# Performance work log

Measured on AMD Instinct MI355X. Metric: run time of the kernel, lower is better.

The kernel has to match this reference:

```python
import jax, jax.numpy as jnp
import numpy as np

N, D, M, E, K = 16384, 512, 1024, 8, 2
LOSS_COEF = 0.01
EPS = 1e-10


def setup_inputs() -> dict:
    key = jax.random.key(0)
    ks = jax.random.split(key, 6)
    x = jax.random.normal(ks[0], (N, D), dtype=jnp.float32)
    # gate weight (torch init is zeros; use small random so routing is non-degenerate)
    w_gate = 0.02 * jax.random.normal(ks[1], (D, E), dtype=jnp.float32)
    # stacked expert FFN params: Linear(D->M), GELU, Linear(M->D)
    W1 = jax.random.normal(ks[2], (E, D, M), dtype=jnp.float32) / np.sqrt(D)
    b1 = jnp.zeros((E, M), dtype=jnp.float32)
    W2 = jax.random.normal(ks[3], (E, M, D), dtype=jnp.float32) / np.sqrt(M)
    b2 = jnp.zeros((E, D), dtype=jnp.float32)
    return {"x": x, "w_gate": w_gate, "W1": W1, "b1": b1, "W2": W2, "b2": b2}


def _cv_squared(v):
    # torch .var() is unbiased (ddof=1)
    v = v.astype(jnp.float32)
    return jnp.var(v, ddof=1) / (jnp.mean(v) ** 2 + EPS)


def reference(x, w_gate, W1, b1, W2, b2):
    n = x.shape[0]
    # --- noisy_top_k_gating (eval path: no noise) ---
    logits = x @ w_gate                                  # [N, E]
    top_logits, top_idx = jax.lax.top_k(logits, min(K + 1, E))
    topk_logits = top_logits[:, :K]                      # [N, K]
    topk_idx = top_idx[:, :K]                            # [N, K]
    topk_gates = jax.nn.softmax(topk_logits, axis=-1)    # [N, K]
    gates = jnp.zeros_like(logits).at[jnp.arange(n)[:, None], topk_idx].set(topk_gates)
    importance = gates.sum(axis=0)                       # [E]
    load = (gates > 0).sum(axis=0).astype(jnp.float32)   # [E]
    loss = LOSS_COEF * (_cv_squared(importance) + _cv_squared(load))
    # --- experts (dense equivalent of sparse dispatch/combine: gate==0 rows contribute 0) ---
    h = jnp.einsum('nd,edm->enm', x, W1) + b1[:, None, :]     # [E, N, M]
    h = jax.nn.gelu(h, approximate=False)
    out = jnp.einsum('enm,emd->end', h, W2) + b2[:, None, :]  # [E, N, D]
    y = jnp.einsum('ne,end->nd', gates, out)                  # [N, D]
    return (y, loss)
```

## Files before the change

kernel.cpp:

```cpp
#include <hip/hip_runtime.h>
#include <math.h>

#define NTOK 16384
#define DDIM 512
#define MDIM 1024
#define NEXP 8
#define LDSW 32
#define TMAX 264

typedef __attribute__((ext_vector_type(8))) short short8;
typedef __attribute__((ext_vector_type(4))) float floatx4;

__device__ inline unsigned short f2bf(float f){
  union { float f; unsigned int u; } v; v.f = f;
  unsigned int u = v.u;
  u += ((u >> 16) & 1u) + 0x7fffu;
  return (unsigned short)(u >> 16);
}

__device__ inline float bf2f(unsigned short s){
  union { unsigned int u; float f; } v;
  v.u = ((unsigned int)s) << 16;
  return v.f;
}

__device__ inline float gelu_fast(float x){
  float u = x * 0.70710678118654752f;
  float a = fabsf(u);
  float t = __builtin_amdgcn_rcpf(fmaf(0.3275911f, a, 1.0f));
  float p = fmaf(1.061405429f, t, -1.453152027f);
  p = fmaf(p, t, 1.421413741f);
  p = fmaf(p, t, -0.284496736f);
  p = fmaf(p, t, 0.254829592f);
  p = p * t;
  float e = __expf(-u * u);
  float erfa = fmaf(-p, e, 1.0f);
  float erfu = copysignf(erfa, u);
  return 0.5f * x * (1.0f + erfu);
}

__device__ __forceinline__ void gload16(const unsigned short* g, unsigned short* l){
  __builtin_amdgcn_global_load_lds(
      (const __attribute__((address_space(1))) void*)g,
      (__attribute__((address_space(3))) void*)l,
      16, 0, 0);
}


__global__ void init_small_kernel(int* counts, float* imp){
  int t = threadIdx.x;
  if (t < NEXP){ counts[t] = 0; imp[t] = 0.0f; }
}

__global__ void transpose_conv_kernel(const float* __restrict__ in,
                                      unsigned short* __restrict__ out,
                                      int R, int C){
  __shared__ float tile[32][33];
  int e  = blockIdx.z;
  int c0 = blockIdx.x << 5;
  int r0 = blockIdx.y << 5;
  const float* src = in + (size_t)e * R * C;
  unsigned short* dst = out + (size_t)e * R * C;
  int tc = threadIdx.x;
  int tr = threadIdx.y;
  #pragma unroll
  for (int i = 0; i < 32; i += 8)
    tile[tr + i][tc] = src[(size_t)(r0 + tr + i) * C + c0 + tc];
  __syncthreads();
  #pragma unroll
  for (int i = 0; i < 32; i += 8)
    dst[(size_t)(c0 + tr + i) * R + r0 + tc] = f2bf(tile[tc][tr + i]);
}


__global__ __launch_bounds__(256)
void gating_kernel(const float* __restrict__ x,
                   const float* __restrict__ wg,
                   unsigned short* __restrict__ xb,
                   int* __restrict__ tok_e, float* __restrict__ tok_g,
                   int* __restrict__ counts, float* __restrict__ imp){
  __shared__ int   lcnt[NEXP];
  __shared__ float limp[NEXP];
  int t = threadIdx.x;
  if (t < NEXP){ lcnt[t] = 0; limp[t] = 0.0f; }
  __syncthreads();

  int wave = t >> 6;
  int lane = t & 63;

  for (int it = 0; it < 16; it++){
    int n = blockIdx.x * 64 + it * 4 + wave;

    const float4* xp = (const float4*)(x + (size_t)n * DDIM + lane * 8);
    float4 a = xp[0], b = xp[1];
    float xv[8] = {a.x, a.y, a.z, a.w, b.x, b.y, b.z, b.w};

    short8 xo;
    #pragma unroll
    for (int j = 0; j < 8; j++) xo[j] = (short)f2bf(xv[j]);
    *(short8*)(xb + (size_t)n * DDIM + lane * 8) = xo;

    double acc[NEXP];
    #pragma unroll
    for (int e = 0; e < NEXP; e++) acc[e] = 0.0;
    #pragma unroll
    for (int j = 0; j < 8; j++){
      const float* wr = wg + (size_t)(lane * 8 + j) * NEXP;
      #pragma unroll
      for (int e = 0; e < NEXP; e++) acc[e] += (double)xv[j] * (double)wr[e];
    }
    #pragma unroll
    for (int off = 32; off >= 1; off >>= 1){
      #pragma unroll
      for (int e = 0; e < NEXP; e++) acc[e] += __shfl_xor(acc[e], off);
    }
    if (lane == 0){
      int i0 = -1, i1 = -1;
      double l0 = -1e300, l1 = -1e300;
      #pragma unroll
      for (int e = 0; e < NEXP; e++){
        double v = acc[e];
        if (v > l0){ l1 = l0; i1 = i0; l0 = v; i0 = e; }
        else if (v > l1){ l1 = v; i1 = e; }
      }
      float ex = expf((float)(l1 - l0));
      float g0 = 1.0f / (1.0f + ex);
      float g1 = ex / (1.0f + ex);
      tok_e[n * 2]     = i0; tok_e[n * 2 + 1] = i1;
      tok_g[n * 2]     = g0; tok_g[n * 2 + 1] = g1;
      atomicAdd(&lcnt[i0], 1); atomicAdd(&lcnt[i1], 1);
      atomicAdd(&limp[i0], g0); atomicAdd(&limp[i1], g1);
    }
  }
  __syncthreads();
  if (t < NEXP){
    atomicAdd(&counts[t], lcnt[t]);
    atomicAdd(&imp[t], limp[t]);
  }
}

__global__ void loss_scan_kernel(const int* __restrict__ counts,
                                 const float* __restrict__ imp,
                                 int* __restrict__ offsets, int* __restrict__ cursor,
                                 int* __restrict__ tile_pre,
                                 float* __restrict__ out_loss){
  int off = 0, tp = 0;
  double si = 0, si2 = 0, sl = 0, sl2 = 0;
  for (int e = 0; e < NEXP; e++){
    offsets[e] = off; cursor[e] = off;
    tile_pre[e] = tp;
    tp += (counts[e] + 127) >> 7;
    off += counts[e];
    double im = (double)imp[e];
    double ld = (double)counts[e];
    si += im; si2 += im * im;
    sl += ld; sl2 += ld * ld;
  }
  offsets[NEXP] = off;
  tile_pre[NEXP] = tp;
  double mi = si / 8.0, ml = sl / 8.0;
  double vi = (si2 - 8.0 * mi * mi) / 7.0;
  double vl = (sl2 - 8.0 * ml * ml) / 7.0;
  double loss = 0.01 * (vi / (mi * mi + 1e-10) + vl / (ml * ml + 1e-10));
  *out_loss = (float)loss;
}

__global__ __launch_bounds__(256)
void scatter_kernel(const int* __restrict__ tok_e,
                    int* __restrict__ cursor,
                    int* __restrict__ btok, int* __restrict__ slot_of){
  __shared__ int lcnt[NEXP];
  __shared__ int lbase[NEXP];
  int t = threadIdx.x;
  if (t < NEXP) lcnt[t] = 0;
  __syncthreads();

  int n = blockIdx.x * 256 + t;
  int e0 = tok_e[n * 2], e1 = tok_e[n * 2 + 1];
  int r0 = atomicAdd(&lcnt[e0], 1);
  int r1 = atomicAdd(&lcnt[e1], 1);
  __syncthreads();
  if (t < NEXP) lbase[t] = atomicAdd(&cursor[t], lcnt[t]);
  __syncthreads();
  int s0 = lbase[e0] + r0;
  int s1 = lbase[e1] + r1;
  btok[s0] = n;
  btok[s1] = n;
  slot_of[n * 2]     = s0;
  slot_of[n * 2 + 1] = s1;
}


__global__ __launch_bounds__(256)
void gemm1_kernel(const unsigned short* __restrict__ xb,
                  const unsigned short* __restrict__ w1t,
                  const float* __restrict__ b1,
                  const int* __restrict__ offsets,
                  const int* __restrict__ tile_pre,
                  const int* __restrict__ btok,
                  unsigned short* __restrict__ H){
  int ct = blockIdx.x / TMAX;
  int tt = blockIdx.x % TMAX;
  if (tt >= tile_pre[NEXP]) return;
  int e = 0;
  while (tt >= tile_pre[e + 1]) e++;
  int rt = tt - tile_pre[e];
  int off = offsets[e];
  int cnt = offsets[e + 1] - off;
  int r0 = rt << 7;

  __shared__ unsigned short As[128 * LDSW];
  __shared__ unsigned short Bs[128 * LDSW];

  int t = threadIdx.x;
  int srow = t >> 2;
  int scol = (t & 3) << 3;
  int w = t >> 6;

  int ra0 = r0 + srow;        if (ra0 >= cnt) ra0 = cnt - 1;
  int ra1 = r0 + 64 + srow;   if (ra1 >= cnt) ra1 = cnt - 1;
  const unsigned short* aptr0 = xb + (size_t)btok[off + ra0] * DDIM + scol;
  const unsigned short* aptr1 = xb + (size_t)btok[off + ra1] * DDIM + scol;
  const unsigned short* bptr0 = w1t + ((size_t)e * MDIM + (ct << 7) + srow) * DDIM + scol;
  const unsigned short* bptr1 = bptr0 + (size_t)64 * DDIM;

  unsigned short* As0 = As + w * 512;
  unsigned short* As1 = As + 2048 + w * 512;
  unsigned short* Bs0 = Bs + w * 512;
  unsigned short* Bs1 = Bs + 2048 + w * 512;

  int lane = t & 63;
  int wr = (w >> 1) << 6;
  int wc = (w & 1) << 6;
  int lm = lane & 15;
  int lq = lane >> 4;

  const unsigned short* Ar[4];
  const unsigned short* Br[4];
  #pragma unroll
  for (int i = 0; i < 4; i++){
    Ar[i] = &As[(wr + i * 16 + lm) * LDSW + lq * 8];
    Br[i] = &Bs[(wc + i * 16 + lm) * LDSW + lq * 8];
  }

  floatx4 acc[4][4] = {};
  for (int k0 = 0; k0 < DDIM; k0 += 32){
    gload16(aptr0 + k0, As0);
    gload16(aptr1 + k0, As1);
    gload16(bptr0 + k0, Bs0);
    gload16(bptr1 + k0, Bs1);
    __syncthreads();
    short8 af[4], bf[4];
    #pragma unroll
    for (int i = 0; i < 4; i++) af[i] = *(const short8*)Ar[i];
    #pragma unroll
    for (int j = 0; j < 4; j++) bf[j] = *(const short8*)Br[j];
    #pragma unroll
    for (int i = 0; i < 4; i++)
      #pragma unroll
      for (int j = 0; j < 4; j++)
        acc[i][j] = __builtin_amdgcn_mfma_f32_16x16x32_bf16(af[i], bf[j], acc[i][j], 0, 0, 0);
    __syncthreads();
  }

  const float* bias = b1 + e * MDIM + (ct << 7);
  #pragma unroll
  for (int i = 0; i < 4; i++){
    int rbase = wr + i * 16 + lq * 4;
    #pragma unroll
    for (int j = 0; j < 4; j++){
      int cc = wc + j * 16 + lm;
      float bv = bias[cc];
      #pragma unroll
      for (int r = 0; r < 4; r++){
        int row = r0 + rbase + r;
        if (row < cnt){
          float v = acc[i][j][r] + bv;
          H[(size_t)(off + row) * MDIM + (ct << 7) + cc] = f2bf(gelu_fast(v));
        }
      }
    }
  }
}

__global__ __launch_bounds__(256)
void gemm2_kernel(const unsigned short* __restrict__ H,
                  const unsigned short* __restrict__ w2t,
                  const float* __restrict__ b2,
                  const int* __restrict__ offsets,
                  const int* __restrict__ tile_pre,
                  unsigned short* __restrict__ O){
  int ct = blockIdx.x / TMAX;
  int tt = blockIdx.x % TMAX;
  if (tt >= tile_pre[NEXP]) return;
  int e = 0;
  while (tt >= tile_pre[e + 1]) e++;
  int rt = tt - tile_pre[e];
  int off = offsets[e];
  int cnt = offsets[e + 1] - off;
  int r0 = rt << 7;

  __shared__ unsigned short As[128 * LDSW];
  __shared__ unsigned short Bs[128 * LDSW];

  int t = threadIdx.x;
  int srow = t >> 2;
  int scol = (t & 3) << 3;
  int w = t >> 6;

  int ra0 = r0 + srow;        if (ra0 >= cnt) ra0 = cnt - 1;
  int ra1 = r0 + 64 + srow;   if (ra1 >= cnt) ra1 = cnt - 1;
  const unsigned short* aptr0 = H + (size_t)(off + ra0) * MDIM + scol;
  const unsigned short* aptr1 = H + (size_t)(off + ra1) * MDIM + scol;
  const unsigned short* bptr0 = w2t + ((size_t)e * DDIM + (ct << 7) + srow) * MDIM + scol;
  const unsigned short* bptr1 = bptr0 + (size_t)64 * MDIM;

  unsigned short* As0 = As + w * 512;
  unsigned short* As1 = As + 2048 + w * 512;
  unsigned short* Bs0 = Bs + w * 512;
  unsigned short* Bs1 = Bs + 2048 + w * 512;

  int lane = t & 63;
  int wr = (w >> 1) << 6;
  int wc = (w & 1) << 6;
  int lm = lane & 15;
  int lq = lane >> 4;

  const unsigned short* Ar[4];
  const unsigned short* Br[4];
  #pragma unroll
  for (int i = 0; i < 4; i++){
    Ar[i] = &As[(wr + i * 16 + lm) * LDSW + lq * 8];
    Br[i] = &Bs[(wc + i * 16 + lm) * LDSW + lq * 8];
  }

  floatx4 acc[4][4] = {};
  for (int k0 = 0; k0 < MDIM; k0 += 32){
    gload16(aptr0 + k0, As0);
    gload16(aptr1 + k0, As1);
    gload16(bptr0 + k0, Bs0);
    gload16(bptr1 + k0, Bs1);
    __syncthreads();
    short8 af[4], bf[4];
    #pragma unroll
    for (int i = 0; i < 4; i++) af[i] = *(const short8*)Ar[i];
    #pragma unroll
    for (int j = 0; j < 4; j++) bf[j] = *(const short8*)Br[j];
    #pragma unroll
    for (int i = 0; i < 4; i++)
      #pragma unroll
      for (int j = 0; j < 4; j++)
        acc[i][j] = __builtin_amdgcn_mfma_f32_16x16x32_bf16(af[i], bf[j], acc[i][j], 0, 0, 0);
    __syncthreads();
  }

  const float* bias = b2 + e * DDIM + (ct << 7);
  #pragma unroll
  for (int i = 0; i < 4; i++){
    int rbase = wr + i * 16 + lq * 4;
    #pragma unroll
    for (int j = 0; j < 4; j++){
      int cc = wc + j * 16 + lm;
      float bv = bias[cc];
      #pragma unroll
      for (int r = 0; r < 4; r++){
        int row = r0 + rbase + r;
        if (row < cnt)
          O[(size_t)(off + row) * DDIM + (ct << 7) + cc] = f2bf(acc[i][j][r] + bv);
      }
    }
  }
}


__global__ __launch_bounds__(256)
void combine_kernel(const unsigned short* __restrict__ O,
                    const float* __restrict__ tok_g,
                    const int* __restrict__ slot_of,
                    float* __restrict__ y){
  int wave = threadIdx.x >> 6;
  int lane = threadIdx.x & 63;
  int n = blockIdx.x * 4 + wave;
  int s0 = slot_of[n * 2], s1 = slot_of[n * 2 + 1];
  float g0 = tok_g[n * 2], g1 = tok_g[n * 2 + 1];
  short8 a = *(const short8*)(O + (size_t)s0 * DDIM + lane * 8);
  short8 b = *(const short8*)(O + (size_t)s1 * DDIM + lane * 8);
  float4 o0, o1;
  float* po0 = (float*)&o0;
  float* po1 = (float*)&o1;
  #pragma unroll
  for (int j = 0; j < 4; j++){
    po0[j] = g0 * bf2f((unsigned short)a[j]) + g1 * bf2f((unsigned short)b[j]);
    po1[j] = g0 * bf2f((unsigned short)a[j + 4]) + g1 * bf2f((unsigned short)b[j + 4]);
  }
  float4* yp = (float4*)(y + (size_t)n * DDIM + lane * 8);
  yp[0] = o0;
  yp[1] = o1;
}


extern "C" void kernel_launch(void* const* d_in, const int* in_sizes, int n_in,
                              void* d_out, int out_size, void* d_ws, size_t ws_size,
                              hipStream_t stream){
  const float* x  = (const float*)d_in[0];
  const float* wg = (const float*)d_in[1];
  const float* W1 = (const float*)d_in[2];
  const float* b1 = (const float*)d_in[3];
  const float* W2 = (const float*)d_in[4];
  const float* b2 = (const float*)d_in[5];
  float* y = (float*)d_out;

  char* ws = (char*)d_ws;
  size_t o = 0;
  auto alloc = [&](size_t bytes)->char*{
    char* p = ws + o;
    o += (bytes + 255) & ~(size_t)255;
    return p;
  };
  unsigned short* xb   = (unsigned short*)alloc((size_t)NTOK * DDIM * 2);
  unsigned short* w1t  = (unsigned short*)alloc((size_t)NEXP * MDIM * DDIM * 2);
  unsigned short* w2t  = (unsigned short*)alloc((size_t)NEXP * DDIM * MDIM * 2);
  unsigned short* H    = (unsigned short*)alloc((size_t)NTOK * 2 * MDIM * 2);
  unsigned short* O    = (unsigned short*)alloc((size_t)NTOK * 2 * DDIM * 2);
  int*   btok    = (int*)  alloc((size_t)NTOK * 2 * 4);
  int*   slot_of = (int*)  alloc((size_t)NTOK * 2 * 4);
  int*   tok_e   = (int*)  alloc((size_t)NTOK * 2 * 4);
  float* tok_g   = (float*)alloc((size_t)NTOK * 2 * 4);
  int*   counts  = (int*)  alloc(64);
  float* imp     = (float*)alloc(64);
  int*   offsets = (int*)  alloc(64);
  int*   cursor  = (int*)  alloc(64);
  int*   tile_pre= (int*)  alloc(64);

  hipLaunchKernelGGL(init_small_kernel, dim3(1), dim3(64), 0, stream, counts, imp);
  hipLaunchKernelGGL(transpose_conv_kernel, dim3(MDIM / 32, DDIM / 32, NEXP), dim3(32, 8), 0, stream,
                     W1, w1t, DDIM, MDIM);
  hipLaunchKernelGGL(transpose_conv_kernel, dim3(DDIM / 32, MDIM / 32, NEXP), dim3(32, 8), 0, stream,
                     W2, w2t, MDIM, DDIM);
  hipLaunchKernelGGL(gating_kernel, dim3(NTOK / 64), dim3(256), 0, stream,
                     x, wg, xb, tok_e, tok_g, counts, imp);
  hipLaunchKernelGGL(loss_scan_kernel, dim3(1), dim3(1), 0, stream,
                     counts, imp, offsets, cursor, tile_pre, y + (size_t)NTOK * DDIM);
  hipLaunchKernelGGL(scatter_kernel, dim3(NTOK / 256), dim3(256), 0, stream,
                     tok_e, cursor, btok, slot_of);
  hipLaunchKernelGGL(gemm1_kernel, dim3(TMAX * 8), dim3(256), 0, stream,
                     xb, w1t, b1, offsets, tile_pre, btok, H);
  hipLaunchKernelGGL(gemm2_kernel, dim3(TMAX * 4), dim3(256), 0, stream,
                     H, w2t, b2, offsets, tile_pre, O);
  hipLaunchKernelGGL(combine_kernel, dim3(NTOK / 4), dim3(256), 0, stream,
                     O, tok_g, slot_of, y);
}
```

Baseline: 308.6 us.

## Double K-step per barrier and vectorize epilogue stores via swapped MFMA operands

Both expert GEMM kernels now stage 64 K-elements per iteration in two LDS halves, which halves the number of barrier pairs per tile. The MFMA operands are swapped so each lane holds four consecutive output columns instead of four rows. That lets the epilogue load bias as a float4 and write four packed bf16 values with one 8-byte store rather than scattered 2-byte stores. The cost is double the LDS footprint per block, which may reduce occupancy.

```diff
diff --git a/kernel.cpp b/kernel.cpp
--- a/kernel.cpp
+++ b/kernel.cpp
@@ -5,7 +5,6 @@
 #define DDIM 512
 #define MDIM 1024
 #define NEXP 8
-#define LDSW 32
 #define TMAX 264
 
 typedef __attribute__((ext_vector_type(8))) short short8;
@@ -209,8 +208,10 @@
   int cnt = offsets[e + 1] - off;
   int r0 = rt << 7;
 
-  __shared__ unsigned short As[128 * LDSW];
-  __shared__ unsigned short Bs[128 * LDSW];
+  __shared__ unsigned short AsLo[128 * 32];
+  __shared__ unsigned short AsHi[128 * 32];
+  __shared__ unsigned short BsLo[128 * 32];
+  __shared__ unsigned short BsHi[128 * 32];
 
   int t = threadIdx.x;
   int srow = t >> 2;
@@ -224,61 +225,58 @@
   const unsigned short* bptr0 = w1t + ((size_t)e * MDIM + (ct << 7) + srow) * DDIM + scol;
   const unsigned short* bptr1 = bptr0 + (size_t)64 * DDIM;
 
-  unsigned short* As0 = As + w * 512;
-  unsigned short* As1 = As + 2048 + w * 512;
-  unsigned short* Bs0 = Bs + w * 512;
-  unsigned short* Bs1 = Bs + 2048 + w * 512;
-
   int lane = t & 63;
   int wr = (w >> 1) << 6;
   int wc = (w & 1) << 6;
   int lm = lane & 15;
   int lq = lane >> 4;
 
-  const unsigned short* Ar[4];
-  const unsigned short* Br[4];
+  floatx4 acc[4][4] = {};
+  for (int k0 = 0; k0 < DDIM; k0 += 64){
+    gload16(aptr0 + k0,      AsLo + w * 512);
+    gload16(aptr0 + k0 + 32, AsHi + w * 512);
+    gload16(aptr1 + k0,      AsLo + 2048 + w * 512);
+    gload16(aptr1 + k0 + 32, AsHi + 2048 + w * 512);
+    gload16(bptr0 + k0,      BsLo + w * 512);
+    gload16(bptr0 + k0 + 32, BsHi + w * 512);
+    gload16(bptr1 + k0,      BsLo + 2048 + w * 512);
+    gload16(bptr1 + k0 + 32, BsHi + 2048 + w * 512);
+    __syncthreads();
+    #pragma unroll
+    for (int h = 0; h < 2; h++){
+      const unsigned short* Ap = h ? AsHi : AsLo;
+      const unsigned short* Bp = h ? BsHi : BsLo;
+      short8 af[4], bf[4];
+      #pragma unroll
+      for (int i = 0; i < 4; i++) af[i] = *(const short8*)&Ap[(wr + i * 16 + lm) * 32 + lq * 8];
+      #pragma unroll
+      for (int j = 0; j < 4; j++) bf[j] = *(const short8*)&Bp[(wc + j * 16 + lm) * 32 + lq * 8];
+      #pragma unroll
+      for (int i = 0; i < 4; i++)
+        #pragma unroll
+        for (int j = 0; j < 4; j++)
+          acc[i][j] = __builtin_amdgcn_mfma_f32_16x16x32_bf16(bf[j], af[i], acc[i][j], 0, 0, 0);
+    }
+    __syncthreads();
+  }
+
+  const float* bias = b1 + e * MDIM + (ct << 7) + wc;
   #pragma unroll
   for (int i = 0; i < 4; i++){
-    Ar[i] = &As[(wr + i * 16 + lm) * LDSW + lq * 8];
-    Br[i] = &Bs[(wc + i * 16 + lm) * LDSW + lq * 8];
-  }
-
-  floatx4 acc[4][4] = {};
-  for (int k0 = 0; k0 < DDIM; k0 += 32){
-    gload16(aptr0 + k0, As0);
-    gload16(aptr1 + k0, As1);
-    gload16(bptr0 + k0, Bs0);
-    gload16(bptr1 + k0, Bs1);
-    __syncthreads();
-    short8 af[4], bf[4];
-    #pragma unroll
-    for (int i = 0; i < 4; i++) af[i] = *(const short8*)Ar[i];
-    #pragma unroll
-    for (int j = 0; j < 4; j++) bf[j] = *(const short8*)Br[j];
-    #pragma unroll
-    for (int i = 0; i < 4; i++)
-      #pragma unroll
-      for (int j = 0; j < 4; j++)
-        acc[i][j] = __builtin_amdgcn_mfma_f32_16x16x32_bf16(af[i], bf[j], acc[i][j], 0, 0, 0);
-    __syncthreads();
-  }
-
-  const float* bias = b1 + e * MDIM + (ct << 7);
-  #pragma unroll
-  for (int i = 0; i < 4; i++){
-    int rbase = wr + i * 16 + lq * 4;
+    int tokl = r0 + wr + i * 16 + lm;
+    bool valid = tokl < cnt;
+    unsigned short* hrow = H + (size_t)(off + (valid ? tokl : 0)) * MDIM + (ct << 7) + wc;
     #pragma unroll
     for (int j = 0; j < 4; j++){
-      int cc = wc + j * 16 + lm;
-      float bv = bias[cc];
-      #pragma unroll
-      for (int r = 0; r < 4; r++){
-        int row = r0 + rbase + r;
-        if (row < cnt){
-          float v = acc[i][j][r] + bv;
-          H[(size_t)(off + row) * MDIM + (ct << 7) + cc] = f2bf(gelu_fast(v));
-        }
-      }
+      float4 bv = *(const float4*)(bias + j * 16 + lq * 4);
+      float g0 = gelu_fast(acc[i][j][0] + bv.x);
+      float g1 = gelu_fast(acc[i][j][1] + bv.y);
+      float g2 = gelu_fast(acc[i][j][2] + bv.z);
+      float g3 = gelu_fast(acc[i][j][3] + bv.w);
+      uint2 p;
+      p.x = (unsigned)f2bf(g0) | ((unsigned)f2bf(g1) << 16);
+      p.y = (unsigned)f2bf(g2) | ((unsigned)f2bf(g3) << 16);
+      if (valid) *(uint2*)(hrow + j * 16 + lq * 4) = p;
     }
   }
 }
@@ -300,8 +298,10 @@
   int cnt = offsets[e + 1] - off;
   int r0 = rt << 7;
 
-  __shared__ unsigned short As[128 * LDSW];
-  __shared__ unsigned short Bs[128 * LDSW];
+  __shared__ unsigned short AsLo[128 * 32];
+  __shared__ unsigned short AsHi[128 * 32];
+  __shared__ unsigned short BsLo[128 * 32];
+  __shared__ unsigned short BsHi[128 * 32];
 
   int t = threadIdx.x;
   int srow = t >> 2;
@@ -315,59 +315,54 @@
   const unsigned short* bptr0 = w2t + ((size_t)e * DDIM + (ct << 7) + srow) * MDIM + scol;
   const unsigned short* bptr1 = bptr0 + (size_t)64 * MDIM;
 
-  unsigned short* As0 = As + w * 512;
-  unsigned short* As1 = As + 2048 + w * 512;
-  unsigned short* Bs0 = Bs + w * 512;
-  unsigned short* Bs1 = Bs + 2048 + w * 512;
-
   int lane = t & 63;
   int wr = (w >> 1) << 6;
   int wc = (w & 1) << 6;
   int lm = lane & 15;
   int lq = lane >> 4;
 
-  const unsigned short* Ar[4];
-  const unsigned short* Br[4];
+  floatx4 acc[4][4] = {};
+  for (int k0 = 0; k0 < MDIM; k0 += 64){
+    gload16(aptr0 + k0,      AsLo + w * 512);
+    gload16(aptr0 + k0 + 32, AsHi + w * 512);
+    gload16(aptr1 + k0,      AsLo + 2048 + w * 512);
+    gload16(aptr1 + k0 + 32, AsHi + 2048 + w * 512);
+    gload16(bptr0 + k0,      BsLo + w * 512);
+    gload16(bptr0 + k0 + 32, BsHi + w * 512);
+    gload16(bptr1 + k0,      BsLo + 2048 + w * 512);
+    gload16(bptr1 + k0 + 32, BsHi + 2048 + w * 512);
+    __syncthreads();
+    #pragma unroll
+    for (int h = 0; h < 2; h++){
+      const unsigned short* Ap = h ? AsHi : AsLo;
+      const unsigned short* Bp = h ? BsHi : BsLo;
+      short8 af[4], bf[4];
+      #pragma unroll
+      for (int i = 0; i < 4; i++) af[i] = *(const short8*)&Ap[(wr + i * 16 + lm) * 32 + lq * 8];
+      #pragma unroll
+      for (int j = 0; j < 4; j++) bf[j] = *(const short8*)&Bp[(wc + j * 16 + lm) * 32 + lq * 8];
+      #pragma unroll
+      for (int i = 0; i < 4; i++)
+        #pragma unroll
+        for (int j = 0; j < 4; j++)
+          acc[i][j] = __builtin_amdgcn_mfma_f32_16x16x32_bf16(bf[j], af[i], acc[i][j], 0, 0, 0);
+    }
+    __syncthreads();
+  }
+
+  const float* bias = b2 + e * DDIM + (ct << 7) + wc;
   #pragma unroll
   for (int i = 0; i < 4; i++){
-    Ar[i] = &As[(wr + i * 16 + lm) * LDSW + lq * 8];
-    Br[i] = &Bs[(wc + i * 16 + lm) * LDSW + lq * 8];
-  }
-
-  floatx4 acc[4][4] = {};
-  for (int k0 = 0; k0 < MDIM; k0 += 32){
-    gload16(aptr0 + k0, As0);
-    gload16(aptr1 + k0, As1);
-    gload16(bptr0 + k0, Bs0);
-    gload16(bptr1 + k0, Bs1);
-    __syncthreads();
-    short8 af[4], bf[4];
-    #pragma unroll
-    for (int i = 0; i < 4; i++) af[i] = *(const short8*)Ar[i];
-    #pragma unroll
-    for (int j = 0; j < 4; j++) bf[j] = *(const short8*)Br[j];
-    #pragma unroll
-    for (int i = 0; i < 4; i++)
-      #pragma unroll
-      for (int j = 0; j < 4; j++)
-        acc[i][j] = __builtin_amdgcn_mfma_f32_16x16x32_bf16(af[i], bf[j], acc[i][j], 0, 0, 0);
-    __syncthreads();
-  }
-
-  const float* bias = b2 + e * DDIM + (ct << 7);
-  #pragma unroll
-  for (int i = 0; i < 4; i++){
-    int rbase = wr + i * 16 + lq * 4;
+    int tokl = r0 + wr + i * 16 + lm;
+    bool valid = tokl < cnt;
+    unsigned short* orow = O + (size_t)(off + (valid ? tokl : 0)) * DDIM + (ct << 7) + wc;
     #pragma unroll
     for (int j = 0; j < 4; j++){
-      int cc = wc + j * 16 + lm;
-      float bv = bias[cc];
-      #pragma unroll
-      for (int r = 0; r < 4; r++){
-        int row = r0 + rbase + r;
-        if (row < cnt)
-          O[(size_t)(off + row) * DDIM + (ct << 7) + cc] = f2bf(acc[i][j][r] + bv);
-      }
+      float4 bv = *(const float4*)(bias + j * 16 + lq * 4);
+      uint2 p;
+      p.x = (unsigned)f2bf(acc[i][j][0] + bv.x) | ((unsigned)f2bf(acc[i][j][1] + bv.y) << 16);
+      p.y = (unsigned)f2bf(acc[i][j][2] + bv.z) | ((unsigned)f2bf(acc[i][j][3] + bv.w) << 16);
+      if (valid) *(uint2*)(orow + j * 16 + lq * 4) = p;
     }
   }
 }
```

Measured after the change: 309.5 us. About the same (+0.3%).
